# Optimization experiments

Measured on AMD Instinct MI355X. Metric: run time of the kernel, lower is better.

The kernel has to match this reference:

```python
import jax, jax.numpy as jnp
import numpy as np

D_MODEL = 1024
NUM_HEADS = 16
D_K = D_MODEL // NUM_HEADS
THETA = 10000.0


def _rope(x, pos):
    # x: [B, H, S, D_K], pos: [S]
    angles = 1.0 / (THETA ** (jnp.arange(0, D_K, 2, dtype=jnp.float32) / D_K))  # [D_K/2]
    ang = pos.astype(jnp.float32)[:, None] * angles  # [S, D_K/2]
    cos = jnp.repeat(jnp.cos(ang), 2, axis=-1)  # [S, D_K]
    sin = jnp.repeat(jnp.sin(ang), 2, axis=-1)
    x2 = x.reshape(*x.shape[:-1], D_K // 2, 2)
    xr = jnp.stack([-x2[..., 1], x2[..., 0]], axis=-1).reshape(x.shape)
    return x * cos + xr * sin


def setup_inputs() -> dict:
    key = jax.random.key(0)
    ks = jax.random.split(key, 5)
    B, S = 2, 2048
    sd = np.sqrt(2.0 / (D_MODEL + D_MODEL))
    return {
        "x": jax.random.normal(ks[0], (B, S, D_MODEL), dtype=jnp.float32),
        "token_positions": jnp.arange(S, dtype=jnp.int32),
        "Wq": jax.random.normal(ks[1], (D_MODEL, D_MODEL), dtype=jnp.float32) * sd,
        "Wk": jax.random.normal(ks[2], (D_MODEL, D_MODEL), dtype=jnp.float32) * sd,
        "Wv": jax.random.normal(ks[3], (D_MODEL, D_MODEL), dtype=jnp.float32) * sd,
        "Wo": jax.random.normal(ks[4], (D_MODEL, D_MODEL), dtype=jnp.float32) * sd,
    }


def reference(x, token_positions, Wq, Wk, Wv, Wo):
    B, S, _ = x.shape

    def proj_heads(W):
        y = jnp.einsum('bsd,ed->bse', x, W)  # weight stored [d_out, d_in]
        return y.reshape(B, S, NUM_HEADS, D_K).transpose(0, 2, 1, 3)  # [B,H,S,Dk]

    q = _rope(proj_heads(Wq), token_positions)
    k = _rope(proj_heads(Wk), token_positions)
    v = proj_heads(Wv)

    scores = jnp.einsum('bhqd,bhkd->bhqk', q, k) / np.sqrt(D_K)  # [B,H,S,S]
    causal = jnp.tril(jnp.ones((S, S), dtype=bool))
    scores = jnp.where(causal, scores, -jnp.inf)
    attn = jax.nn.softmax(scores, axis=-1)
    out = jnp.einsum('bhqk,bhkd->bhqd', attn, v)  # [B,H,S,Dk]
    out = out.transpose(0, 2, 1, 3).reshape(B, S, D_MODEL)
    return jnp.einsum('bsd,ed->bse', out, Wo)
```

## Files before the change

kernel.cpp:

```cpp
#include <hip/hip_runtime.h>
#include <hip/hip_bf16.h>
#include <cstdint>
#include <cmath>

#define SEQ 2048
#define NH 16
#define DM 1024
#define BATCH 2

typedef short bf16x8 __attribute__((ext_vector_type(8)));
typedef float f32x4 __attribute__((ext_vector_type(4)));
typedef const void __attribute__((address_space(1)))* gas_t;
typedef void __attribute__((address_space(3)))* las_t;

#if __has_builtin(__builtin_amdgcn_exp2f)
#define EXP2(x) __builtin_amdgcn_exp2f(x)
#else
#define EXP2(x) __expf((x) * 0.6931471805599453f)
#endif

#define QSCALE 0.18033688011112042f

static __device__ __forceinline__ unsigned short f2bf(float f) {
    union { __hip_bfloat16 h; unsigned short u; } cv;
    cv.h = __float2bfloat16(f);
    return cv.u;
}
static __device__ __forceinline__ float bf2f(unsigned short u) {
    union { unsigned short u; __hip_bfloat16 h; } cv;
    cv.u = u;
    return __bfloat162float(cv.h);
}

static __device__ __forceinline__ void gload_lds16(const void* g, void* l) {
    __builtin_amdgcn_global_load_lds(
        reinterpret_cast<gas_t>(reinterpret_cast<uintptr_t>(g)),
        reinterpret_cast<las_t>(reinterpret_cast<uintptr_t>(l)),
        16, 0, 0);
}

__global__ __launch_bounds__(256) void cvt_all(
    const float* __restrict__ x,  const float* __restrict__ wq,
    const float* __restrict__ wk, const float* __restrict__ wv,
    const float* __restrict__ wo,
    unsigned short* __restrict__ xb, unsigned short* __restrict__ wqkv,
    unsigned short* __restrict__ wob) {
    int blk = blockIdx.x;
    const float* src; unsigned short* dst; int base;
    if (blk < 4096)      { src = x;  dst = xb;              base = blk; }
    else if (blk < 5120) { src = wq; dst = wqkv;            base = blk - 4096; }
    else if (blk < 6144) { src = wk; dst = wqkv + 1048576;  base = blk - 5120; }
    else if (blk < 7168) { src = wv; dst = wqkv + 2097152;  base = blk - 6144; }
    else                 { src = wo; dst = wob;             base = blk - 7168; }
    int i = base * 256 + threadIdx.x;
    float4 v = reinterpret_cast<const float4*>(src)[i];
    ushort4 o;
    o.x = f2bf(v.x); o.y = f2bf(v.y); o.z = f2bf(v.z); o.w = f2bf(v.w);
    reinterpret_cast<ushort4*>(dst)[i] = o;
}

template<int OUT_BF16>
__global__ __launch_bounds__(256) void gemm_bt(
    const unsigned short* __restrict__ A,
    const unsigned short* __restrict__ B,
    void* __restrict__ C, int M, int N, int K) {
    __shared__ unsigned short As[128 * 32];
    __shared__ unsigned short Bs[128 * 32];
    const int tid = threadIdx.x;
    const int lane = tid & 63, wid = tid >> 6;
    const int wr = wid >> 1, wc = wid & 1;
    const int ln15 = lane & 15, kq = lane >> 4;
    const int bm = blockIdx.y, bn = blockIdx.x;

    f32x4 acc[4][4] = {};
    const int nk = K >> 5;
    for (int kt = 0; kt < nk; ++kt) {
        #pragma unroll
        for (int i = 0; i < 2; ++i) {
            int c = i * 256 + tid;
            int row = c >> 2, k8 = (c & 3) << 3;
            size_t gofsA = (size_t)(bm * 128 + row) * K + kt * 32 + k8;
            size_t gofsB = (size_t)(bn * 128 + row) * K + kt * 32 + k8;
            unsigned ldsoff = (unsigned)(i * 256 + wid * 64) * 16;
            gload_lds16(A + gofsA, (char*)As + ldsoff);
            gload_lds16(B + gofsB, (char*)Bs + ldsoff);
        }
        __syncthreads();
        bf16x8 af[4], bf[4];
        #pragma unroll
        for (int m = 0; m < 4; ++m)
            af[m] = *reinterpret_cast<const bf16x8*>(&As[(wr * 64 + m * 16 + ln15) * 32 + kq * 8]);
        #pragma unroll
        for (int n = 0; n < 4; ++n)
            bf[n] = *reinterpret_cast<const bf16x8*>(&Bs[(wc * 64 + n * 16 + ln15) * 32 + kq * 8]);
        #pragma unroll
        for (int m = 0; m < 4; ++m)
            #pragma unroll
            for (int n = 0; n < 4; ++n)
                acc[m][n] = __builtin_amdgcn_mfma_f32_16x16x32_bf16(af[m], bf[n], acc[m][n], 0, 0, 0);
        __syncthreads();
    }
    #pragma unroll
    for (int m = 0; m < 4; ++m) {
        #pragma unroll
        for (int n = 0; n < 4; ++n) {
            int col = bn * 128 + wc * 64 + n * 16 + ln15;
            #pragma unroll
            for (int j = 0; j < 4; ++j) {
                int row = bm * 128 + wr * 64 + m * 16 + kq * 4 + j;
                if constexpr (OUT_BF16 != 0)
                    ((unsigned short*)C)[(size_t)row * N + col] = f2bf(acc[m][n][j]);
                else
                    ((float*)C)[(size_t)row * N + col] = acc[m][n][j];
            }
        }
    }
}

__global__ __launch_bounds__(512) void gemm256_bt(
    const unsigned short* __restrict__ A,
    const unsigned short* __restrict__ B,
    unsigned short* __restrict__ C, int M, int N, int K) {
    __shared__ unsigned short As[2][256 * 64];
    __shared__ unsigned short Bs[2][256 * 64];
    const int tid = threadIdx.x;
    const int lane = tid & 63, wid = tid >> 6;
    const int wm = wid >> 2, wn = wid & 3;
    const int ln15 = lane & 15, g = lane >> 4;
    const int bm = blockIdx.y, bn = blockIdx.x;

    const unsigned short* aSrc[4];
    const unsigned short* bSrc[4];
    #pragma unroll
    for (int p = 0; p < 4; ++p) {
        int c = tid + (p << 9);
        int row = c >> 3, slot = c & 7;
        aSrc[p] = A + (size_t)(bm * 256 + row) * K + ((slot ^ (row & 7)) << 3);
        bSrc[p] = B + (size_t)(bn * 256 + row) * K + ((slot ^ (row & 7)) << 3);
    }
    auto stageA = [&](int kt, int h) {
        #pragma unroll
        for (int p = 2 * h; p < 2 * h + 2; ++p) {
            unsigned dst = (unsigned)(tid + (p << 9)) << 4;
            gload_lds16(aSrc[p] + kt * 64, (char*)As[kt & 1] + dst);
        }
    };
    auto stageB = [&](int kt, int h) {
        #pragma unroll
        for (int p = 2 * h; p < 2 * h + 2; ++p) {
            unsigned dst = (unsigned)(tid + (p << 9)) << 4;
            gload_lds16(bSrc[p] + kt * 64, (char*)Bs[kt & 1] + dst);
        }
    };

    const unsigned ps0 = (unsigned)((g ^ (ln15 & 7)) << 4);
    const unsigned ps1 = (unsigned)(((4 + g) ^ (ln15 & 7)) << 4);
    const unsigned aBase = (unsigned)(wm * 128 + ln15) * 128;
    const unsigned bBase = (unsigned)(wn * 64 + ln15) * 128;

    f32x4 acc[8][4] = {};
    const int nkt = K >> 6;
    const int nit = nkt >> 1;

    stageA(0, 0); stageA(0, 1);
    stageB(0, 0); stageB(0, 1);
    stageB(1, 0); stageB(1, 1);
    asm volatile("s_waitcnt vmcnt(0)" ::: "memory");
    __builtin_amdgcn_s_barrier();

    for (int j = 0; j < nit; ++j) {
        const int t0 = 2 * j, t1 = 2 * j + 1;
        const bool more = (t0 + 2) < nkt;
        #pragma unroll
        for (int grp = 0; grp < 2; ++grp) {
            const char* Ab = (const char*)As[grp];
            const char* Bb = (const char*)Bs[grp];
            bf16x8 bfr[4][2];
            #pragma unroll
            for (int q = 0; q < 4; ++q) {
                if (q == 0) {
                    #pragma unroll
                    for (int nf = 0; nf < 4; ++nf) {
                        bfr[nf][0] = *reinterpret_cast<const bf16x8*>(Bb + bBase + nf * 2048 + ps0);
                        bfr[nf][1] = *reinterpret_cast<const bf16x8*>(Bb + bBase + nf * 2048 + ps1);
                    }
                }
                bf16x8 af0 = *reinterpret_cast<const bf16x8*>(Ab + aBase + (2 * q) * 2048 + ps0);
                bf16x8 af1 = *reinterpret_cast<const bf16x8*>(Ab + aBase + (2 * q) * 2048 + ps1);
                bf16x8 af2 = *reinterpret_cast<const bf16x8*>(Ab + aBase + (2 * q + 1) * 2048 + ps0);
                bf16x8 af3 = *reinterpret_cast<const bf16x8*>(Ab + aBase + (2 * q + 1) * 2048 + ps1);

                if (grp == 0) {
                    if (q == 0) stageA(t1, 0);
                    else if (q == 1) stageA(t1, 1);
                    else if (q == 2) { if (more) stageB(t0 + 2, 0); }
                    else {
                        if (more) { stageB(t0 + 2, 1);
                                    asm volatile("s_waitcnt vmcnt(4)" ::: "memory"); }
                        else      { asm volatile("s_waitcnt vmcnt(0)" ::: "memory"); }
                    }
                } else {
                    if (q == 0)      { if (more) stageA(t0 + 2, 0); }
                    else if (q == 1) { if (more) stageA(t0 + 2, 1); }
                    else if (q == 2) { if (more) stageB(t1 + 2, 0); }
                    else {
                        if (more) { stageB(t1 + 2, 1);
                                    asm volatile("s_waitcnt vmcnt(4)" ::: "memory"); }
                        else      { asm volatile("s_waitcnt vmcnt(0)" ::: "memory"); }
                    }
                }

                __builtin_amdgcn_s_barrier();
                asm volatile("s_waitcnt lgkmcnt(0)" ::: "memory");
                __builtin_amdgcn_s_setprio(1);
                #pragma unroll
                for (int nf = 0; nf < 4; ++nf) {
                    acc[2 * q][nf] = __builtin_amdgcn_mfma_f32_16x16x32_bf16(af0, bfr[nf][0], acc[2 * q][nf], 0, 0, 0);
                    acc[2 * q][nf] = __builtin_amdgcn_mfma_f32_16x16x32_bf16(af1, bfr[nf][1], acc[2 * q][nf], 0, 0, 0);
                    acc[2 * q + 1][nf] = __builtin_amdgcn_mfma_f32_16x16x32_bf16(af2, bfr[nf][0], acc[2 * q + 1][nf], 0, 0, 0);
                    acc[2 * q + 1][nf] = __builtin_amdgcn_mfma_f32_16x16x32_bf16(af3, bfr[nf][1], acc[2 * q + 1][nf], 0, 0, 0);
                }
                __builtin_amdgcn_s_setprio(0);
                __builtin_amdgcn_s_barrier();
            }
        }
    }

    #pragma unroll
    for (int mf = 0; mf < 8; ++mf) {
        #pragma unroll
        for (int nf = 0; nf < 4; ++nf) {
            int col = bn * 256 + wn * 64 + nf * 16 + ln15;
            #pragma unroll
            for (int j = 0; j < 4; ++j) {
                int row = bm * 256 + wm * 128 + mf * 16 + g * 4 + j;
                C[(size_t)row * N + col] = f2bf(acc[mf][nf][j]);
            }
        }
    }
}

__global__ __launch_bounds__(256) void rope_table(const int* __restrict__ pos,
                                                  float2* __restrict__ tab) {
    int idx = blockIdx.x * 256 + threadIdx.x;
    int s = idx >> 5, i = idx & 31;
    float fpos = (float)pos[s];
    float freq = exp2f(-(float)i * (13.287712379549449f / 32.0f));
    float ang = fpos * freq, sn, cs;
    sincosf(ang, &sn, &cs);
    tab[idx] = make_float2(cs, sn);
}

__global__ __launch_bounds__(256) void rope_kernel(
    const unsigned short* __restrict__ qkv, const float2* __restrict__ tab,
    unsigned short* __restrict__ Qh, unsigned short* __restrict__ Kh) {
    int bs = blockIdx.x;
    int b = bs >> 11, s = bs & (SEQ - 1);
    int t = threadIdx.x;
    #pragma unroll
    for (int p = t; p < 512; p += 256) {
        int h = p >> 5, i = p & 31;
        float2 cs = tab[(s << 5) + i];
        size_t src = (size_t)bs * 3072 + h * 64 + 2 * i;
        size_t dst = ((size_t)(b * NH + h) * SEQ + s) * 64 + 2 * i;
        ushort2 qv = *reinterpret_cast<const ushort2*>(qkv + src);
        float q0 = bf2f(qv.x), q1 = bf2f(qv.y);
        ushort2 qo;
        qo.x = f2bf((q0 * cs.x - q1 * cs.y) * QSCALE);
        qo.y = f2bf((q1 * cs.x + q0 * cs.y) * QSCALE);
        *reinterpret_cast<ushort2*>(Qh + dst) = qo;
        ushort2 kv = *reinterpret_cast<const ushort2*>(qkv + src + 1024);
        float k0 = bf2f(kv.x), k1 = bf2f(kv.y);
        ushort2 ko;
        ko.x = f2bf(k0 * cs.x - k1 * cs.y);
        ko.y = f2bf(k1 * cs.x + k0 * cs.y);
        *reinterpret_cast<ushort2*>(Kh + dst) = ko;
    }
}

__global__ __launch_bounds__(256) void vtrans_kernel(
    const unsigned short* __restrict__ qkv, unsigned short* __restrict__ Vo) {
    __shared__ unsigned short tile[64][65];
    int blk = blockIdx.x;
    int st = blk & 31, bh = blk >> 5;
    int sb = st * 64;
    int t = threadIdx.x;
    int b = bh >> 4, h = bh & 15;
    #pragma unroll
    for (int u = t; u < 1024; u += 256) {
        int sl = u >> 4, d4 = (u & 15) << 2;
        ushort4 v = *reinterpret_cast<const ushort4*>(
            qkv + (size_t)(b * SEQ + sb + sl) * 3072 + 2048 + h * 64 + d4);
        tile[sl][d4] = v.x; tile[sl][d4 + 1] = v.y;
        tile[sl][d4 + 2] = v.z; tile[sl][d4 + 3] = v.w;
    }
    __syncthreads();
    #pragma unroll
    for (int u = t; u < 1024; u += 256) {
        int d = u >> 4, s4 = (u & 15) << 2;
        ushort4 o;
        o.x = tile[s4][d]; o.y = tile[s4 + 1][d];
        o.z = tile[s4 + 2][d]; o.w = tile[s4 + 3][d];
        *reinterpret_cast<ushort4*>(Vo + ((size_t)bh * 64 + d) * SEQ + sb + s4) = o;
    }
}

__global__ __launch_bounds__(128) void attn_kernel(
    const unsigned short* __restrict__ Qh, const unsigned short* __restrict__ Kh,
    const unsigned short* __restrict__ Vt, unsigned short* __restrict__ Out) {
    __shared__ unsigned short Kb[2][64 * 64];
    __shared__ unsigned short Vb[2][64 * 64];
    __shared__ unsigned short Plds[2][16 * 72];

    const int tid = threadIdx.x;
    const int wid = tid >> 6, lane = tid & 63;
    const int ln15 = lane & 15, g = lane >> 4;
    const int bid = blockIdx.x;
    const int bh = bid & 31;
    const int pb = bid >> 5;

    const unsigned short* Qp = Qh + (size_t)bh * SEQ * 64;
    const unsigned short* Kp = Kh + (size_t)bh * SEQ * 64;
    const unsigned short* Vp = Vt + (size_t)bh * 64 * SEQ;
    char* Pc = (char*)Plds[wid];

    const unsigned short* kSrc[4];
    const unsigned short* vSrc[4];
    #pragma unroll
    for (int p = 0; p < 4; ++p) {
        int c = tid + (p << 7);
        int row = c >> 3, slot = c & 7;
        kSrc[p] = Kp + (size_t)row * 64 + ((slot ^ (row & 7)) << 3);
        vSrc[p] = Vp + (size_t)row * SEQ + ((slot ^ (row & 7)) << 3);
    }

    auto stage = [&](int kb, int buf) {
        #pragma unroll
        for (int p = 0; p < 4; ++p) {
            unsigned bb = (unsigned)(wid * 1024 + p * 2048);
            gload_lds16(kSrc[p] + (size_t)kb * 64, (char*)Kb[buf] + bb);
            gload_lds16(vSrc[p] + kb, (char*)Vb[buf] + bb);
        }
    };

    unsigned kOff[4][2], vOff[4][2];
    #pragma unroll
    for (int s = 0; s < 4; ++s) {
        int r = ln15 + 16 * s;
        kOff[s][0] = r * 128 + ((g ^ (r & 7)) << 4);
        kOff[s][1] = r * 128 + (((4 + g) ^ (r & 7)) << 4);
    }
    #pragma unroll
    for (int c = 0; c < 4; ++c) {
        int d = c * 16 + ln15;
        vOff[c][0] = d * 128 + ((g ^ (d & 7)) << 4);
        vOff[c][1] = d * 128 + (((4 + g) ^ (d & 7)) << 4);
    }
    const unsigned pW = (unsigned)(ln15 * 144 + 8 * g);
    const unsigned pR = (unsigned)(ln15 * 144 + 16 * g);

    const int b = bh >> 4, h = bh & 15;

    for (int bi = 0; bi < 2; ++bi) {
        const int bnd = bi ? (63 - pb) : pb;
        const int qb = bnd * 32 + wid * 16;
        const int nt = (bnd + 2) >> 1;
        const int thr = qb + ln15 - 4 * g;

        bf16x8 aq0 = *reinterpret_cast<const bf16x8*>(Qp + (size_t)(qb + ln15) * 64 + g * 8);
        bf16x8 aq1 = *reinterpret_cast<const bf16x8*>(Qp + (size_t)(qb + ln15) * 64 + 32 + g * 8);

        f32x4 oacc[4] = {};
        float lsum = 0.f;

        stage(0, 0);

        for (int t = 0; t < nt; ++t) {
            const int kb = t << 6;
            const int cur = t & 1;
            if (t + 1 < nt) {
                stage((t + 1) << 6, cur ^ 1);
                asm volatile("s_waitcnt vmcnt(8)" ::: "memory");
            } else {
                asm volatile("s_waitcnt vmcnt(0)" ::: "memory");
            }
            __builtin_amdgcn_s_barrier();

            const char* K0 = (const char*)Kb[cur];
            const char* V0 = (const char*)Vb[cur];
            bf16x8 kf[8], bv[8];
            #pragma unroll
            for (int s = 0; s < 4; ++s) {
                kf[2 * s]     = *reinterpret_cast<const bf16x8*>(K0 + kOff[s][0]);
                kf[2 * s + 1] = *reinterpret_cast<const bf16x8*>(K0 + kOff[s][1]);
            }
            #pragma unroll
            for (int c = 0; c < 4; ++c) {
                bv[2 * c]     = *reinterpret_cast<const bf16x8*>(V0 + vOff[c][0]);
                bv[2 * c + 1] = *reinterpret_cast<const bf16x8*>(V0 + vOff[c][1]);
            }

            const f32x4 z = {};
            f32x4 sq[4];
            #pragma unroll
            for (int s = 0; s < 4; ++s) {
                sq[s] = __builtin_amdgcn_mfma_f32_16x16x32_bf16(kf[2 * s], aq0, z, 0, 0, 0);
                sq[s] = __builtin_amdgcn_mfma_f32_16x16x32_bf16(kf[2 * s + 1], aq1, sq[s], 0, 0, 0);
            }

            float pv[4][4];
            if (t == nt - 1) {
                #pragma unroll
                for (int s = 0; s < 4; ++s)
                    #pragma unroll
                    for (int j = 0; j < 4; ++j)
                        pv[s][j] = (j <= thr - kb - 16 * s) ? EXP2(sq[s][j]) : 0.f;
            } else {
                #pragma unroll
                for (int s = 0; s < 4; ++s)
                    #pragma unroll
                    for (int j = 0; j < 4; ++j)
                        pv[s][j] = EXP2(sq[s][j]);
            }
            #pragma unroll
            for (int s = 0; s < 4; ++s)
                lsum += (pv[s][0] + pv[s][1]) + (pv[s][2] + pv[s][3]);

            #pragma unroll
            for (int s = 0; s < 4; ++s) {
                ushort4 w;
                w.x = f2bf(pv[s][0]); w.y = f2bf(pv[s][1]);
                w.z = f2bf(pv[s][2]); w.w = f2bf(pv[s][3]);
                *reinterpret_cast<ushort4*>(Pc + pW + 32 * s) = w;
            }
            asm volatile("s_waitcnt lgkmcnt(0)" ::: "memory");
            bf16x8 ap0 = *reinterpret_cast<const bf16x8*>(Pc + pR);
            bf16x8 ap1 = *reinterpret_cast<const bf16x8*>(Pc + pR + 64);
            #pragma unroll
            for (int c = 0; c < 4; ++c) {
                oacc[c] = __builtin_amdgcn_mfma_f32_16x16x32_bf16(ap0, bv[2 * c], oacc[c], 0, 0, 0);
                oacc[c] = __builtin_amdgcn_mfma_f32_16x16x32_bf16(ap1, bv[2 * c + 1], oacc[c], 0, 0, 0);
            }
            asm volatile("s_waitcnt lgkmcnt(0)" ::: "memory");
            __builtin_amdgcn_s_barrier();
        }

        float r = lsum;
        r += __shfl_xor(r, 16);
        r += __shfl_xor(r, 32);
        float linv = 1.f / r;
        float invj[4];
        #pragma unroll
        for (int j = 0; j < 4; ++j)
            invj[j] = __shfl(linv, 20 * g + j);
        #pragma unroll
        for (int c = 0; c < 4; ++c)
            #pragma unroll
            for (int j = 0; j < 4; ++j) {
                int s = qb + g * 4 + j;
                Out[((size_t)(b * SEQ + s)) * DM + h * 64 + c * 16 + ln15] =
                    f2bf(oacc[c][j] * invj[j]);
            }
    }
}

extern "C" void kernel_launch(void* const* d_in, const int* in_sizes, int n_in,
                              void* d_out, int out_size, void* d_ws, size_t ws_size,
                              hipStream_t stream) {
    const float* x = (const float*)d_in[0];
    const int* pos = (const int*)d_in[1];
    const float* Wq = (const float*)d_in[2];
    const float* Wk = (const float*)d_in[3];
    const float* Wv = (const float*)d_in[4];
    const float* Wo = (const float*)d_in[5];
    float* out = (float*)d_out;

    char* ws = (char*)d_ws;
    const size_t MB = 1024 * 1024;
    unsigned short* xb   = (unsigned short*)(ws + 0 * MB);
    unsigned short* wqkv = (unsigned short*)(ws + 8 * MB);
    unsigned short* wob  = (unsigned short*)(ws + 14 * MB);
    unsigned short* qkv  = (unsigned short*)(ws + 16 * MB);
    float2*         tab  = (float2*)       (ws + 40 * MB);
    unsigned short* qh   = (unsigned short*)(ws + 41 * MB);
    unsigned short* kh   = (unsigned short*)(ws + 49 * MB);
    unsigned short* vtr  = (unsigned short*)(ws + 57 * MB);
    unsigned short* att  = (unsigned short*)(ws + 65 * MB);

    cvt_all<<<8192, 256, 0, stream>>>(x, Wq, Wk, Wv, Wo, xb, wqkv, wob);
    rope_table<<<256, 256, 0, stream>>>(pos, tab);

    gemm256_bt<<<dim3(12, 16), 512, 0, stream>>>(xb, wqkv, qkv, 4096, 3072, 1024);

    rope_kernel<<<4096, 256, 0, stream>>>(qkv, tab, qh, kh);
    vtrans_kernel<<<1024, 256, 0, stream>>>(qkv, vtr);

    attn_kernel<<<1024, 128, 0, stream>>>(qh, kh, vtr, att);

    gemm_bt<0><<<dim3(8, 32), 256, 0, stream>>>(att, wob, out, 4096, 1024, 1024);
}
```

Baseline: 124.1 us.

## Fuse RoPE and V transpose into QKV GEMM epilogue

The QKV projection GEMM epilogue now applies rotary embedding (with Q scaling) using lane shuffles to fetch the paired element. It writes Q and K directly in head-major layout and writes V transposed, which removes the separate rope and vtrans kernels and the intermediate qkv buffer. This removes two launches and a full write and re-read of the QKV activations. In exchange, the epilogue does scattered 2-byte stores for Q/K plus extra table loads, which may reduce store efficiency.

After: 119.8 us. 1.04x faster.

```diff
diff --git a/kernel.cpp b/kernel.cpp
--- a/kernel.cpp
+++ b/kernel.cpp
@@ -120,7 +120,8 @@
 __global__ __launch_bounds__(512) void gemm256_bt(
     const unsigned short* __restrict__ A,
     const unsigned short* __restrict__ B,
-    unsigned short* __restrict__ C, int M, int N, int K) {
+    unsigned short* __restrict__ Qh, unsigned short* __restrict__ Kh,
+    unsigned short* __restrict__ Vtr, const float2* __restrict__ tab, int K) {
     __shared__ unsigned short As[2][256 * 64];
     __shared__ unsigned short Bs[2][256 * 64];
     const int tid = threadIdx.x;
@@ -226,15 +227,36 @@
         }
     }
 
+    const int sel = bn >> 2;
+    const int colBase = (bn & 3) * 256 + wn * 64;
     #pragma unroll
     for (int mf = 0; mf < 8; ++mf) {
+        int row0 = bm * 256 + wm * 128 + mf * 16 + g * 4;
+        int b = row0 >> 11, s0 = row0 & 2047;
         #pragma unroll
         for (int nf = 0; nf < 4; ++nf) {
-            int col = bn * 256 + wn * 64 + nf * 16 + ln15;
-            #pragma unroll
-            for (int j = 0; j < 4; ++j) {
-                int row = bm * 256 + wm * 128 + mf * 16 + g * 4 + j;
-                C[(size_t)row * N + col] = f2bf(acc[mf][nf][j]);
+            int col = colBase + nf * 16 + ln15;
+            int h = col >> 6, d = col & 63;
+            if (sel == 2) {
+                ushort4 w;
+                w.x = f2bf(acc[mf][nf][0]); w.y = f2bf(acc[mf][nf][1]);
+                w.z = f2bf(acc[mf][nf][2]); w.w = f2bf(acc[mf][nf][3]);
+                *reinterpret_cast<ushort4*>(
+                    &Vtr[(((size_t)(b * NH + h)) * 64 + d) * SEQ + s0]) = w;
+            } else {
+                unsigned short* dst = (sel == 0) ? Qh : Kh;
+                const float sc = (sel == 0) ? QSCALE : 1.f;
+                int i = d >> 1;
+                #pragma unroll
+                for (int j2 = 0; j2 < 4; ++j2) {
+                    float v = acc[mf][nf][j2];
+                    float p = __shfl_xor(v, 1);
+                    float2 cs = tab[((s0 + j2) << 5) + i];
+                    float o = (d & 1) ? (v * cs.x + p * cs.y)
+                                      : (v * cs.x - p * cs.y);
+                    dst[(((size_t)(b * NH + h)) * SEQ + (s0 + j2)) * 64 + d] =
+                        f2bf(o * sc);
+                }
             }
         }
     }
@@ -249,60 +271,6 @@
     float ang = fpos * freq, sn, cs;
     sincosf(ang, &sn, &cs);
     tab[idx] = make_float2(cs, sn);
-}
-
-__global__ __launch_bounds__(256) void rope_kernel(
-    const unsigned short* __restrict__ qkv, const float2* __restrict__ tab,
-    unsigned short* __restrict__ Qh, unsigned short* __restrict__ Kh) {
-    int bs = blockIdx.x;
-    int b = bs >> 11, s = bs & (SEQ - 1);
-    int t = threadIdx.x;
-    #pragma unroll
-    for (int p = t; p < 512; p += 256) {
-        int h = p >> 5, i = p & 31;
-        float2 cs = tab[(s << 5) + i];
-        size_t src = (size_t)bs * 3072 + h * 64 + 2 * i;
-        size_t dst = ((size_t)(b * NH + h) * SEQ + s) * 64 + 2 * i;
-        ushort2 qv = *reinterpret_cast<const ushort2*>(qkv + src);
-        float q0 = bf2f(qv.x), q1 = bf2f(qv.y);
-        ushort2 qo;
-        qo.x = f2bf((q0 * cs.x - q1 * cs.y) * QSCALE);
-        qo.y = f2bf((q1 * cs.x + q0 * cs.y) * QSCALE);
-        *reinterpret_cast<ushort2*>(Qh + dst) = qo;
-        ushort2 kv = *reinterpret_cast<const ushort2*>(qkv + src + 1024);
-        float k0 = bf2f(kv.x), k1 = bf2f(kv.y);
-        ushort2 ko;
-        ko.x = f2bf(k0 * cs.x - k1 * cs.y);
-        ko.y = f2bf(k1 * cs.x + k0 * cs.y);
-        *reinterpret_cast<ushort2*>(Kh + dst) = ko;
-    }
-}
-
-__global__ __launch_bounds__(256) void vtrans_kernel(
-    const unsigned short* __restrict__ qkv, unsigned short* __restrict__ Vo) {
-    __shared__ unsigned short tile[64][65];
-    int blk = blockIdx.x;
-    int st = blk & 31, bh = blk >> 5;
-    int sb = st * 64;
-    int t = threadIdx.x;
-    int b = bh >> 4, h = bh & 15;
-    #pragma unroll
-    for (int u = t; u < 1024; u += 256) {
-        int sl = u >> 4, d4 = (u & 15) << 2;
-        ushort4 v = *reinterpret_cast<const ushort4*>(
-            qkv + (size_t)(b * SEQ + sb + sl) * 3072 + 2048 + h * 64 + d4);
-        tile[sl][d4] = v.x; tile[sl][d4 + 1] = v.y;
-        tile[sl][d4 + 2] = v.z; tile[sl][d4 + 3] = v.w;
-    }
-    __syncthreads();
-    #pragma unroll
-    for (int u = t; u < 1024; u += 256) {
-        int d = u >> 4, s4 = (u & 15) << 2;
-        ushort4 o;
-        o.x = tile[s4][d]; o.y = tile[s4 + 1][d];
-        o.z = tile[s4 + 2][d]; o.w = tile[s4 + 3][d];
-        *reinterpret_cast<ushort4*>(Vo + ((size_t)bh * 64 + d) * SEQ + sb + s4) = o;
-    }
 }
 
 __global__ __launch_bounds__(128) void attn_kernel(
@@ -480,7 +448,6 @@
     unsigned short* xb   = (unsigned short*)(ws + 0 * MB);
     unsigned short* wqkv = (unsigned short*)(ws + 8 * MB);
     unsigned short* wob  = (unsigned short*)(ws + 14 * MB);
-    unsigned short* qkv  = (unsigned short*)(ws + 16 * MB);
     float2*         tab  = (float2*)       (ws + 40 * MB);
     unsigned short* qh   = (unsigned short*)(ws + 41 * MB);
     unsigned short* kh   = (unsigned short*)(ws + 49 * MB);
@@ -490,10 +457,7 @@
     cvt_all<<<8192, 256, 0, stream>>>(x, Wq, Wk, Wv, Wo, xb, wqkv, wob);
     rope_table<<<256, 256, 0, stream>>>(pos, tab);
 
-    gemm256_bt<<<dim3(12, 16), 512, 0, stream>>>(xb, wqkv, qkv, 4096, 3072, 1024);
-
-    rope_kernel<<<4096, 256, 0, stream>>>(qkv, tab, qh, kh);
-    vtrans_kernel<<<1024, 256, 0, stream>>>(qkv, vtr);
+    gemm256_bt<<<dim3(12, 16), 512, 0, stream>>>(xb, wqkv, qh, kh, vtr, tab, 1024);
 
     attn_kernel<<<1024, 128, 0, stream>>>(qh, kh, vtr, att);
 
```
